# Optimization experiments

Measured on AMD Instinct MI355X. Metric: run time of the kernel, lower is better.

Reference implementation:

```python
import jax, jax.numpy as jnp
import numpy as np

V, D, B, C, NEG = 100000, 512, 1024, 20, 64


def setup_inputs() -> dict:
    key = jax.random.key(0)
    k1, k2, k3, k4, k5 = jax.random.split(key, 5)
    center_ids = jax.random.randint(k1, (B,), 0, V)
    context_ids = jax.random.randint(k2, (B, C), 0, V)
    W_center = jax.random.normal(k3, (V, D), dtype=jnp.float32)
    W_context = jax.random.normal(k4, (V, D), dtype=jnp.float32)
    freq = jax.random.uniform(k5, (V,), dtype=jnp.float32, minval=1e-4, maxval=1.0)
    p = freq ** 0.75
    sample_prob = p / p.sum()
    return {
        "center_ids": center_ids,
        "context_ids": context_ids,
        "W_center": W_center,
        "W_context": W_context,
        "sample_prob": sample_prob,
        "neg_sample": NEG,
    }


def _sample_negatives(sample_prob, batch, neg):
    # Gumbel top-k == sampling `neg` items without replacement w.p. proportional to sample_prob.
    log_p = jnp.log(sample_prob)  # [V]
    g = jax.random.gumbel(jax.random.key(42), (batch, sample_prob.shape[0]), dtype=sample_prob.dtype)
    _, idx = jax.lax.top_k(log_p[None, :] + g, neg)  # [B, neg]
    return idx


def reference(center_ids, context_ids, W_center, W_context, sample_prob, neg_sample):
    b, c = context_ids.shape
    embs_center = W_center[center_ids]                    # [B, D]
    # NOTE: original module looks up positive context in the CENTER table (faithful quirk).
    embs_context = W_center[context_ids]                  # [B, C, D]
    neg_idx = _sample_negatives(sample_prob, b, neg_sample)
    embs_negatives = W_context[neg_idx]                   # [B, neg, D]
    cos_positive = jnp.einsum('bcd,bd->bc', embs_context, embs_center)[..., None]   # [B, C, 1]
    cos_negative = jnp.einsum('bnd,bd->bn', embs_negatives, embs_center)[..., None]  # [B, neg, 1]
    return cos_positive, cos_negative
```

## Files before the change

### kernel.cpp

```cpp
#include <hip/hip_runtime.h>
#include <stdint.h>
#include <math.h>

#define V_SZ 100000
#define D_SZ 512
#define B_SZ 1024
#define C_SZ 20
#define NEG 64
#define NB 2048
#define CAP 512
#define ITEMS (C_SZ + NEG)
#define TCUT -5.5451774f

__device__ __forceinline__ float xla_logf(float xin) {
#pragma clang fp contract(off)
  float x = fmaxf(xin, 1.17549435e-38f);
  uint32_t bits = __float_as_uint(x);
  float e = (float)((int)(bits >> 23) - 127) + 1.0f;
  float m = __uint_as_float((bits & 0x807fffffu) | 0x3f000000u);
  bool lt = m < 0.707106781186547524f;
  float tmp = lt ? m : 0.0f;
  m = m - 1.0f;
  e = e - (lt ? 1.0f : 0.0f);
  m = m + tmp;
  float z = m * m;
  float y = 7.0376836292E-2f;
  y = fmaf(y, m, -1.1514610310E-1f);
  y = fmaf(y, m, 1.1676998740E-1f);
  y = fmaf(y, m, -1.2420140846E-1f);
  y = fmaf(y, m, 1.4249322787E-1f);
  y = fmaf(y, m, -1.6668057665E-1f);
  y = fmaf(y, m, 2.0000714765E-1f);
  y = fmaf(y, m, -2.4999993993E-1f);
  y = fmaf(y, m, 3.3333331174E-1f);
  y = y * m;
  y = y * z;
  y = y + e * (-2.12194440e-4f);
  y = y - z * 0.5f;
  x = m + y;
  x = x + e * 0.693359375f;
  return x;
}

__device__ __forceinline__ void threefry2x32(uint32_t x0, uint32_t x1,
                                             uint32_t& o0, uint32_t& o1) {
  const uint32_t ks1 = 42u, ks2 = 0x1BD11BF0u;
#define TFR(r) { x0 += x1; x1 = __builtin_rotateleft32(x1, (r)); x1 ^= x0; }
  x0 += 0u; x1 += ks1;
  TFR(13) TFR(15) TFR(26) TFR(6)
  x0 += ks1; x1 += ks2 + 1u;
  TFR(17) TFR(29) TFR(16) TFR(24)
  x0 += ks2; x1 += 0u + 2u;
  TFR(13) TFR(15) TFR(26) TFR(6)
  x0 += 0u; x1 += ks1 + 3u;
  TFR(17) TFR(29) TFR(16) TFR(24)
  x0 += ks1; x1 += ks2 + 4u;
  TFR(13) TFR(15) TFR(26) TFR(6)
  x0 += ks2; x1 += 0u + 5u;
#undef TFR
  o0 = x0; o1 = x1;
}

__device__ __forceinline__ uint32_t tf_bits_partitionable(uint32_t i) {
  uint32_t o0, o1;
  threefry2x32(0u, i, o0, o1);
  return o0 ^ o1;
}

__device__ __forceinline__ float gumbel_from_bits(uint32_t bits) {
#pragma clang fp contract(off)
  float f = __uint_as_float((bits >> 9) | 0x3f800000u) - 1.0f;
  float u = (bits >> 9) ? f : 1.17549435e-38f;
  return -xla_logf(-xla_logf(u));
}

__device__ __forceinline__ float score_one(uint32_t i, float lpv) {
#pragma clang fp contract(off)
  return lpv + gumbel_from_bits(tf_bits_partitionable(i));
}

__global__ __launch_bounds__(256) void compute_thr(const float* __restrict__ sp,
                                                   uint32_t* __restrict__ thr_pre) {
  int v = blockIdx.x * 256 + threadIdx.x;
  if (v >= V_SZ) return;
  float lpv = xla_logf(sp[v]);
  float need = TCUT - lpv;
  float u = expf(-expf(-need));
  int m = (int)floorf(u * 8388608.0f) - 128;
  thr_pre[v] = ((uint32_t)(m < 0 ? 0 : m)) << 9;
}

__global__ __launch_bounds__(256) void select_negs(const float* __restrict__ sp,
                                                   const uint32_t* __restrict__ thr_pre,
                                                   int* __restrict__ negidx) {
  __shared__ uint32_t hist[NB];
  __shared__ float    cs[CAP];
  __shared__ int      ci[CAP];
  __shared__ uint32_t cb[CAP];
  __shared__ int      cnt;
  __shared__ int      cnt_hi;
  __shared__ int      cut;

  const int b = blockIdx.x;
  const uint32_t base = (uint32_t)b * (uint32_t)V_SZ;

  if (threadIdx.x == 0) { cnt = 0; cnt_hi = 0; }
  __syncthreads();

#pragma unroll 2
  for (int v = threadIdx.x; v < V_SZ; v += 256) {
    uint32_t bits = tf_bits_partitionable(base + (uint32_t)v);
    if (bits >= thr_pre[v]) {
      int k = atomicAdd(&cnt, 1);
      if (k < CAP) { ci[k] = v; cb[k] = bits; }
    }
  }
  __syncthreads();

  int n0 = min(cnt, CAP);
  for (int i = threadIdx.x; i < n0; i += 256) {
    float s = xla_logf(sp[ci[i]]) + gumbel_from_bits(cb[i]);
    cs[i] = s;
    if (s >= TCUT) atomicAdd(&cnt_hi, 1);
  }
  __syncthreads();

  if (cnt <= CAP && cnt_hi >= NEG) {
    int n = cnt;
    for (int i = threadIdx.x; i < n; i += 256) {
      float si = cs[i]; int vi = ci[i];
      int rank = 0;
      for (int j = 0; j < n; ++j) {
        float sj = cs[j];
        rank += (sj > si) || (sj == si && ci[j] < vi);
      }
      if (rank < NEG) negidx[b * NEG + rank] = vi;
    }
    return;
  }

  const float LO = -28.0f, INVW = 51.2f;
  for (int i = threadIdx.x; i < NB; i += 256) hist[i] = 0u;
  if (threadIdx.x == 0) cnt = 0;
  __syncthreads();

  for (int v = threadIdx.x; v < V_SZ; v += 256) {
    float s = score_one(base + (uint32_t)v, xla_logf(sp[v]));
    int bin = min(NB - 1, max(0, (int)((s - LO) * INVW)));
    atomicAdd(&hist[bin], 1u);
  }
  __syncthreads();

  if (threadIdx.x == 0) {
    uint32_t acc = 0; int c = NB - 1;
    for (; c > 0; --c) { acc += hist[c]; if (acc >= (uint32_t)NEG) break; }
    cut = c;
  }
  __syncthreads();
  const int cutb = cut;

  for (int v = threadIdx.x; v < V_SZ; v += 256) {
    float s = score_one(base + (uint32_t)v, xla_logf(sp[v]));
    int bin = min(NB - 1, max(0, (int)((s - LO) * INVW)));
    if (bin >= cutb) {
      int k = atomicAdd(&cnt, 1);
      if (k < CAP) { cs[k] = s; ci[k] = v; }
    }
  }
  __syncthreads();

  int n = min(cnt, CAP);
  for (int i = threadIdx.x; i < n; i += 256) {
    float si = cs[i]; int vi = ci[i];
    int rank = 0;
    for (int j = 0; j < n; ++j) {
      float sj = cs[j];
      rank += (sj > si) || (sj == si && ci[j] < vi);
    }
    if (rank < NEG) negidx[b * NEG + rank] = vi;
  }
}

__global__ __launch_bounds__(256) void dots(const int* __restrict__ center_ids,
                                            const int* __restrict__ context_ids,
                                            const float* __restrict__ Wcen,
                                            const float* __restrict__ Wctx,
                                            const int* __restrict__ negidx,
                                            float* __restrict__ out) {
  const int wid  = blockIdx.x * 4 + (threadIdx.x >> 6);
  const int lane = threadIdx.x & 63;
  const int b = wid / ITEMS;
  const int j = wid - b * ITEMS;

  const float4* crow = (const float4*)(Wcen + (size_t)center_ids[b] * D_SZ);
  const float* row;
  if (j < C_SZ) row = Wcen + (size_t)context_ids[b * C_SZ + j] * D_SZ;
  else          row = Wctx + (size_t)negidx[b * NEG + (j - C_SZ)] * D_SZ;
  const float4* r4 = (const float4*)row;

  float4 a0 = r4[lane * 2];
  float4 a1 = r4[lane * 2 + 1];
  float4 c0 = crow[lane * 2];
  float4 c1 = crow[lane * 2 + 1];

  float p = a0.x * c0.x + a0.y * c0.y + a0.z * c0.z + a0.w * c0.w +
            a1.x * c1.x + a1.y * c1.y + a1.z * c1.z + a1.w * c1.w;
  for (int off = 32; off; off >>= 1) p += __shfl_xor(p, off, 64);

  if (lane == 0) {
    if (j < C_SZ) out[b * C_SZ + j] = p;
    else          out[B_SZ * C_SZ + b * NEG + (j - C_SZ)] = p;
  }
}

extern "C" void kernel_launch(void* const* d_in, const int* in_sizes, int n_in,
                              void* d_out, int out_size, void* d_ws, size_t ws_size,
                              hipStream_t stream) {
  (void)in_sizes; (void)n_in; (void)out_size; (void)ws_size;
  const int*   center_ids  = (const int*)d_in[0];
  const int*   context_ids = (const int*)d_in[1];
  const float* Wcen        = (const float*)d_in[2];
  const float* Wctx        = (const float*)d_in[3];
  const float* sp          = (const float*)d_in[4];

  uint32_t* thr_pre = (uint32_t*)d_ws;
  int*      negidx  = (int*)((char*)d_ws + 512 * 1024);

  compute_thr<<<(V_SZ + 255) / 256, 256, 0, stream>>>(sp, thr_pre);
  select_negs<<<B_SZ,              256, 0, stream>>>(sp, thr_pre, negidx);
  dots       <<<(B_SZ * ITEMS) / 4, 256, 0, stream>>>(center_ids, context_ids,
                                                      Wcen, Wctx, negidx,
                                                      (float*)d_out);
}
```

Before: 654.9 us.

## Batch four Threefry counters per thread, widen selection blocks, and group dot products

The candidate scan in select_negs now computes four consecutive Threefry counters per thread with interleaved rounds and loads four thresholds as one vector. Selection blocks grow from 256 to 512 threads. The dots kernel has each wavefront handle four items for the same batch row, so the center row is loaded once per four dots and more row loads are in flight. The aim is more instruction-level parallelism in the RNG-bound scan and less redundant center-row traffic, at the cost of higher register pressure.

Result: faster. 619.8 us (-5.4%).

```diff
diff --git a/kernel.cpp b/kernel.cpp
--- a/kernel.cpp
+++ b/kernel.cpp
@@ -9,6 +9,7 @@
 #define NEG 64
 #define NB 2048
 #define CAP 512
+#define TPB 512
 #define ITEMS (C_SZ + NEG)
 #define TCUT -5.5451774f
 
@@ -67,6 +68,31 @@
   return o0 ^ o1;
 }
 
+__device__ __forceinline__ void threefry4(uint32_t c0, uint32_t out[4]) {
+  const uint32_t ks1 = 42u, ks2 = 0x1BD11BF0u;
+  uint32_t a[4], b[4];
+#pragma unroll
+  for (int k = 0; k < 4; ++k) { a[k] = 0u; b[k] = c0 + (uint32_t)k + ks1; }
+#define R4(r) { _Pragma("unroll") for (int k = 0; k < 4; ++k) { \
+    a[k] += b[k]; b[k] = __builtin_rotateleft32(b[k], (r)); b[k] ^= a[k]; } }
+#define INJ(i0, i1) { _Pragma("unroll") for (int k = 0; k < 4; ++k) { \
+    a[k] += (i0); b[k] += (i1); } }
+  R4(13) R4(15) R4(26) R4(6)
+  INJ(ks1, ks2 + 1u)
+  R4(17) R4(29) R4(16) R4(24)
+  INJ(ks2, 0u + 2u)
+  R4(13) R4(15) R4(26) R4(6)
+  INJ(0u, ks1 + 3u)
+  R4(17) R4(29) R4(16) R4(24)
+  INJ(ks1, ks2 + 4u)
+  R4(13) R4(15) R4(26) R4(6)
+  INJ(ks2, 0u + 5u)
+#undef R4
+#undef INJ
+#pragma unroll
+  for (int k = 0; k < 4; ++k) out[k] = a[k] ^ b[k];
+}
+
 __device__ __forceinline__ float gumbel_from_bits(uint32_t bits) {
 #pragma clang fp contract(off)
   float f = __uint_as_float((bits >> 9) | 0x3f800000u) - 1.0f;
@@ -90,7 +116,7 @@
   thr_pre[v] = ((uint32_t)(m < 0 ? 0 : m)) << 9;
 }
 
-__global__ __launch_bounds__(256) void select_negs(const float* __restrict__ sp,
+__global__ __launch_bounds__(TPB) void select_negs(const float* __restrict__ sp,
                                                    const uint32_t* __restrict__ thr_pre,
                                                    int* __restrict__ negidx) {
   __shared__ uint32_t hist[NB];
@@ -107,18 +133,19 @@
   if (threadIdx.x == 0) { cnt = 0; cnt_hi = 0; }
   __syncthreads();
 
-#pragma unroll 2
-  for (int v = threadIdx.x; v < V_SZ; v += 256) {
-    uint32_t bits = tf_bits_partitionable(base + (uint32_t)v);
-    if (bits >= thr_pre[v]) {
-      int k = atomicAdd(&cnt, 1);
-      if (k < CAP) { ci[k] = v; cb[k] = bits; }
-    }
+  for (int v0 = threadIdx.x * 4; v0 < V_SZ; v0 += TPB * 4) {
+    uint32_t bits[4];
+    threefry4(base + (uint32_t)v0, bits);
+    uint4 t4 = *(const uint4*)(thr_pre + v0);
+    if (bits[0] >= t4.x) { int k = atomicAdd(&cnt, 1); if (k < CAP) { ci[k] = v0;     cb[k] = bits[0]; } }
+    if (bits[1] >= t4.y) { int k = atomicAdd(&cnt, 1); if (k < CAP) { ci[k] = v0 + 1; cb[k] = bits[1]; } }
+    if (bits[2] >= t4.z) { int k = atomicAdd(&cnt, 1); if (k < CAP) { ci[k] = v0 + 2; cb[k] = bits[2]; } }
+    if (bits[3] >= t4.w) { int k = atomicAdd(&cnt, 1); if (k < CAP) { ci[k] = v0 + 3; cb[k] = bits[3]; } }
   }
   __syncthreads();
 
   int n0 = min(cnt, CAP);
-  for (int i = threadIdx.x; i < n0; i += 256) {
+  for (int i = threadIdx.x; i < n0; i += TPB) {
     float s = xla_logf(sp[ci[i]]) + gumbel_from_bits(cb[i]);
     cs[i] = s;
     if (s >= TCUT) atomicAdd(&cnt_hi, 1);
@@ -127,7 +154,7 @@
 
   if (cnt <= CAP && cnt_hi >= NEG) {
     int n = cnt;
-    for (int i = threadIdx.x; i < n; i += 256) {
+    for (int i = threadIdx.x; i < n; i += TPB) {
       float si = cs[i]; int vi = ci[i];
       int rank = 0;
       for (int j = 0; j < n; ++j) {
@@ -140,11 +167,11 @@
   }
 
   const float LO = -28.0f, INVW = 51.2f;
-  for (int i = threadIdx.x; i < NB; i += 256) hist[i] = 0u;
+  for (int i = threadIdx.x; i < NB; i += TPB) hist[i] = 0u;
   if (threadIdx.x == 0) cnt = 0;
   __syncthreads();
 
-  for (int v = threadIdx.x; v < V_SZ; v += 256) {
+  for (int v = threadIdx.x; v < V_SZ; v += TPB) {
     float s = score_one(base + (uint32_t)v, xla_logf(sp[v]));
     int bin = min(NB - 1, max(0, (int)((s - LO) * INVW)));
     atomicAdd(&hist[bin], 1u);
@@ -159,7 +186,7 @@
   __syncthreads();
   const int cutb = cut;
 
-  for (int v = threadIdx.x; v < V_SZ; v += 256) {
+  for (int v = threadIdx.x; v < V_SZ; v += TPB) {
     float s = score_one(base + (uint32_t)v, xla_logf(sp[v]));
     int bin = min(NB - 1, max(0, (int)((s - LO) * INVW)));
     if (bin >= cutb) {
@@ -170,7 +197,7 @@
   __syncthreads();
 
   int n = min(cnt, CAP);
-  for (int i = threadIdx.x; i < n; i += 256) {
+  for (int i = threadIdx.x; i < n; i += TPB) {
     float si = cs[i]; int vi = ci[i];
     int rank = 0;
     for (int j = 0; j < n; ++j) {
@@ -187,29 +214,39 @@
                                             const float* __restrict__ Wctx,
                                             const int* __restrict__ negidx,
                                             float* __restrict__ out) {
-  const int wid  = blockIdx.x * 4 + (threadIdx.x >> 6);
+  const int q    = blockIdx.x * 4 + (threadIdx.x >> 6);
   const int lane = threadIdx.x & 63;
-  const int b = wid / ITEMS;
-  const int j = wid - b * ITEMS;
+  const int b  = q / 21;
+  const int jj = q - b * 21;
+  const int j0 = jj * 4;
 
   const float4* crow = (const float4*)(Wcen + (size_t)center_ids[b] * D_SZ);
-  const float* row;
-  if (j < C_SZ) row = Wcen + (size_t)context_ids[b * C_SZ + j] * D_SZ;
-  else          row = Wctx + (size_t)negidx[b * NEG + (j - C_SZ)] * D_SZ;
-  const float4* r4 = (const float4*)row;
-
-  float4 a0 = r4[lane * 2];
-  float4 a1 = r4[lane * 2 + 1];
+  const float4* r4[4];
+#pragma unroll
+  for (int u = 0; u < 4; ++u) {
+    int j = j0 + u;
+    const float* row;
+    if (j < C_SZ) row = Wcen + (size_t)context_ids[b * C_SZ + j] * D_SZ;
+    else          row = Wctx + (size_t)negidx[b * NEG + (j - C_SZ)] * D_SZ;
+    r4[u] = (const float4*)row;
+  }
+
   float4 c0 = crow[lane * 2];
   float4 c1 = crow[lane * 2 + 1];
-
-  float p = a0.x * c0.x + a0.y * c0.y + a0.z * c0.z + a0.w * c0.w +
-            a1.x * c1.x + a1.y * c1.y + a1.z * c1.z + a1.w * c1.w;
-  for (int off = 32; off; off >>= 1) p += __shfl_xor(p, off, 64);
-
-  if (lane == 0) {
-    if (j < C_SZ) out[b * C_SZ + j] = p;
-    else          out[B_SZ * C_SZ + b * NEG + (j - C_SZ)] = p;
+  float4 a0[4], a1[4];
+#pragma unroll
+  for (int u = 0; u < 4; ++u) { a0[u] = r4[u][lane * 2]; a1[u] = r4[u][lane * 2 + 1]; }
+
+#pragma unroll
+  for (int u = 0; u < 4; ++u) {
+    float p = a0[u].x * c0.x + a0[u].y * c0.y + a0[u].z * c0.z + a0[u].w * c0.w +
+              a1[u].x * c1.x + a1[u].y * c1.y + a1[u].z * c1.z + a1[u].w * c1.w;
+    for (int off = 32; off; off >>= 1) p += __shfl_xor(p, off, 64);
+    if (lane == 0) {
+      int j = j0 + u;
+      if (j < C_SZ) out[b * C_SZ + j] = p;
+      else          out[B_SZ * C_SZ + b * NEG + (j - C_SZ)] = p;
+    }
   }
 }
 
@@ -227,8 +264,8 @@
   int*      negidx  = (int*)((char*)d_ws + 512 * 1024);
 
   compute_thr<<<(V_SZ + 255) / 256, 256, 0, stream>>>(sp, thr_pre);
-  select_negs<<<B_SZ,              256, 0, stream>>>(sp, thr_pre, negidx);
-  dots       <<<(B_SZ * ITEMS) / 4, 256, 0, stream>>>(center_ids, context_ids,
-                                                      Wcen, Wctx, negidx,
-                                                      (float*)d_out);
-}
+  select_negs<<<B_SZ,              TPB, 0, stream>>>(sp, thr_pre, negidx);
+  dots       <<<(B_SZ * ITEMS) / 16, 256, 0, stream>>>(center_ids, context_ids,
+                                                       Wcen, Wctx, negidx,
+                                                       (float*)d_out);
+}
```
